# Kernel optimization log

Measured on AMD Instinct MI355X. Metric: run time of the kernel, lower is better.

The kernel has to match this reference:

```python
import jax, jax.numpy as jnp
import numpy as np

B, S, D = 2, 4096, 1024
E, H, TOPK = 8, 2736, 2


def setup_inputs() -> dict:
    key = jax.random.key(0)
    k_x, k_g, k_wg, k_w1, k_w2 = jax.random.split(key, 5)
    scale = 0.02
    return {
        "x": jax.random.normal(k_x, (B, S, D), dtype=jnp.float32),
        "gate_w": jax.random.normal(k_g, (E, D), dtype=jnp.float32) * scale,
        "Wg": jax.random.normal(k_wg, (E, H, D), dtype=jnp.float32) * scale,
        "W1": jax.random.normal(k_w1, (E, H, D), dtype=jnp.float32) * scale,
        "W2": jax.random.normal(k_w2, (E, D, H), dtype=jnp.float32) * scale,
    }


def reference(x, gate_w, Wg, W1, W2):
    C = x.shape[-1]
    xf = x.reshape(-1, C)                     # [T, D], T = B*S tokens
    # --- TopKRouter (eval mode: no jitter) ---
    logits = xf @ gate_w.T                    # [T, E]
    probs = jax.nn.softmax(logits.astype(jnp.float32), axis=-1)
    top_p, top_i = jax.lax.top_k(probs, TOPK)          # [T, K]
    gate_weights = top_p / (top_p.sum(axis=-1, keepdims=True) + 1e-8)
    # combine weight per (token, expert): sum of gate weights over selected slots
    combine = jnp.sum(jax.nn.one_hot(top_i, E, dtype=xf.dtype) * gate_weights[..., None], axis=1)  # [T, E]
    # --- SwiGLU experts, weighted combine ---
    out = jnp.zeros_like(xf)
    for e in range(E):  # fixed small expert count; GEMMs dominate
        g = jax.nn.silu(xf @ Wg[e].T)         # [T, H]
        up = xf @ W1[e].T                     # [T, H]
        y = (g * up) @ W2[e].T                # [T, D]
        out = out + combine[:, e:e + 1] * y
    return out.reshape(x.shape)
```

## Files before the change

kernel.cpp:

```cpp
#include <hip/hip_runtime.h>
#include <hip/hip_bf16.h>
#include <stdint.h>

#define T_TOK 8192
#define DIM   1024
#define NEXP  8
#define HDIM  2736
#define HPAD  2816
#define CAP   16384
#define HB_ROWS 17408

typedef __attribute__((ext_vector_type(8))) short          short8;
typedef __attribute__((ext_vector_type(8))) unsigned short ushort8;
typedef __attribute__((ext_vector_type(4))) float          f32x4;

__device__ __forceinline__ unsigned short f2bf(float f) {
  unsigned u = __float_as_uint(f);
  u = (u + 0x7FFFu + ((u >> 16) & 1u)) >> 16;
  return (unsigned short)u;
}

__device__ __forceinline__ void gld_lds16(const ushort* g, ushort* l) {
  __builtin_amdgcn_global_load_lds((const __attribute__((address_space(1))) uint32_t*)g,
                                   (__attribute__((address_space(3))) uint32_t*)l,
                                   16, 0, 0);
}

__device__ __forceinline__ void stage64(const ushort* __restrict__ src, int ldK,
                                        ushort* lds, int tid) {
#pragma unroll
  for (int i = 0; i < 4; ++i) {
    int c = i * 256 + tid;
    int row = c >> 3, col8 = c & 7;
    gld_lds16(src + (size_t)row * ldK + col8 * 8,
              lds + (size_t)(i * 256 + (tid & 192)) * 8);
  }
}

__global__ void cvt_x_kernel(const float* __restrict__ in, ushort* __restrict__ out, int n8) {
  int i = blockIdx.x * 256 + threadIdx.x;
  if (i >= n8) return;
  const float4* p = (const float4*)in + (size_t)i * 2;
  float4 a = p[0], b = p[1];
  ushort8 v;
  v[0]=f2bf(a.x); v[1]=f2bf(a.y); v[2]=f2bf(a.z); v[3]=f2bf(a.w);
  v[4]=f2bf(b.x); v[5]=f2bf(b.y); v[6]=f2bf(b.z); v[7]=f2bf(b.w);
  ((ushort8*)out)[i] = v;
}

__global__ void cvt_pad_rows_kernel(const float* __restrict__ in, ushort* __restrict__ out, int n8) {
  int i = blockIdx.x * 256 + threadIdx.x;
  if (i >= n8) return;
  int col = i & 127;
  int rowAll = i >> 7;
  int e = rowAll / HPAD;
  int r = rowAll - e * HPAD;
  ushort8 v = (ushort8)0;
  if (r < HDIM) {
    const float4* p = (const float4*)(in + ((size_t)(e * HDIM + r) * DIM + col * 8));
    float4 a = p[0], b = p[1];
    v[0]=f2bf(a.x); v[1]=f2bf(a.y); v[2]=f2bf(a.z); v[3]=f2bf(a.w);
    v[4]=f2bf(b.x); v[5]=f2bf(b.y); v[6]=f2bf(b.z); v[7]=f2bf(b.w);
  }
  ((ushort8*)out)[i] = v;
}

__global__ void cvt_pad_inner_kernel(const float* __restrict__ in, ushort* __restrict__ out, int n8) {
  int i = blockIdx.x * 256 + threadIdx.x;
  if (i >= n8) return;
  int h8 = HPAD / 8;
  int c = i % h8;
  int rowAll = i / h8;
  int h0 = c * 8;
  ushort8 v = (ushort8)0;
  if (h0 < HDIM) {
    const float4* p = (const float4*)(in + (size_t)rowAll * HDIM + h0);
    float4 a = p[0], b = p[1];
    v[0]=f2bf(a.x); v[1]=f2bf(a.y); v[2]=f2bf(a.z); v[3]=f2bf(a.w);
    v[4]=f2bf(b.x); v[5]=f2bf(b.y); v[6]=f2bf(b.z); v[7]=f2bf(b.w);
  }
  ((ushort8*)out)[i] = v;
}

__global__ void topk_kernel(const float* __restrict__ X, const float* __restrict__ GW,
                            int* __restrict__ sel0, int* __restrict__ sel1,
                            float* __restrict__ w0, float* __restrict__ w1) {
  int wave = threadIdx.x >> 6, lane = threadIdx.x & 63;
  int t = blockIdx.x * 4 + wave;
  if (t >= T_TOK) return;
  float acc[NEXP];
#pragma unroll
  for (int e = 0; e < NEXP; ++e) acc[e] = 0.f;
  const float4* xv = (const float4*)(X + (size_t)t * DIM);
#pragma unroll
  for (int it = 0; it < DIM / 4 / 64; ++it) {
    int c = it * 64 + lane;
    float4 xx = xv[c];
#pragma unroll
    for (int e = 0; e < NEXP; ++e) {
      float4 w = ((const float4*)(GW + (size_t)e * DIM))[c];
      acc[e] += xx.x * w.x + xx.y * w.y + xx.z * w.z + xx.w * w.w;
    }
  }
#pragma unroll
  for (int e = 0; e < NEXP; ++e)
#pragma unroll
    for (int off = 32; off > 0; off >>= 1)
      acc[e] += __shfl_down(acc[e], off, 64);
  if (lane == 0) {
    float m = acc[0];
#pragma unroll
    for (int e = 1; e < NEXP; ++e) m = fmaxf(m, acc[e]);
    float p[NEXP], s = 0.f;
#pragma unroll
    for (int e = 0; e < NEXP; ++e) { p[e] = expf(acc[e] - m); s += p[e]; }
#pragma unroll
    for (int e = 0; e < NEXP; ++e) p[e] /= s;
    int i0 = 0;
#pragma unroll
    for (int e = 1; e < NEXP; ++e) if (p[e] > p[i0]) i0 = e;
    int i1 = (i0 == 0) ? 1 : 0;
#pragma unroll
    for (int e = 0; e < NEXP; ++e) if (e != i0 && p[e] > p[i1]) i1 = e;
    float denom = p[i0] + p[i1] + 1e-8f;
    sel0[t] = i0; sel1[t] = i1;
    w0[t] = p[i0] / denom;
    w1[t] = p[i1] / denom;
  }
}

__global__ __launch_bounds__(1024) void build_lists_kernel(
    const int* __restrict__ sel0, const int* __restrict__ sel1,
    int* __restrict__ tok, int* __restrict__ rnk0, int* __restrict__ rnk1,
    int* __restrict__ cnt) {
  int e = blockIdx.x;
  int tid = threadIdx.x;
  int lane = tid & 63, wv = tid >> 6;
  __shared__ int wsum[16], wbase[16], chunktot;
  int base = 0;
  for (int t0 = 0; t0 < T_TOK; t0 += 1024) {
    int t = t0 + tid;
    int s0 = sel0[t], s1 = sel1[t];
    bool isf = (s0 == e);
    bool hit = isf || (s1 == e);
    unsigned long long b = __ballot(hit);
    int rank = __popcll(b & ((1ULL << lane) - 1ULL));
    if (lane == 0) wsum[wv] = __popcll(b);
    __syncthreads();
    if (tid == 0) {
      int s = 0;
#pragma unroll
      for (int w = 0; w < 16; ++w) { wbase[w] = s; s += wsum[w]; }
      chunktot = s;
    }
    __syncthreads();
    if (hit) {
      int pos = base + wbase[wv] + rank;
      tok[e * CAP + pos] = t;
      if (isf) rnk0[t] = pos; else rnk1[t] = pos;
    }
    base += chunktot;
    __syncthreads();
  }
  if (tid == 0) cnt[e] = base;
}

__global__ void offsets_kernel(const int* __restrict__ cnt, int* __restrict__ off) {
  if (threadIdx.x == 0 && blockIdx.x == 0) {
    int o = 0;
#pragma unroll
    for (int e = 0; e < NEXP; ++e) { off[e] = o; o += (cnt[e] + 127) & ~127; }
    off[NEXP] = o;
  }
}

__global__ __launch_bounds__(256) void gemm1_all_kernel(
    const ushort* __restrict__ X,
    const ushort* __restrict__ Wgb,
    const ushort* __restrict__ Wub,
    ushort* __restrict__ Hout,
    const int* __restrict__ tokall,
    const int* __restrict__ cntv, const int* __restrict__ offv) {
  int row0 = blockIdx.x * 128;
  if (row0 >= offv[NEXP]) return;
  int e = 0;
#pragma unroll
  for (int k = 1; k < NEXP; ++k) if (row0 >= offv[k]) e = k;
  int local = row0 - offv[e];
  int cnt = cntv[e];
  const int* tokl = tokall + (size_t)e * CAP;

  __shared__ ushort As[2][128 * 32];
  __shared__ ushort Bg[2][128 * 32];
  __shared__ ushort Bu[2][128 * 32];
  int tid = threadIdx.x;
  int lane = tid & 63, wave = tid >> 6;
  int wr = wave >> 1, wc = wave & 1;
  int lhi = lane >> 4, llo = lane & 15;
  int bcol = blockIdx.y * 128;
  int ldsoff = tid & 192;

  const ushort* asrc[2];
#pragma unroll
  for (int i = 0; i < 2; ++i) {
    int p = local + (tid >> 2) + 64 * i;
    int t = (p < cnt) ? tokl[p] : 0;
    asrc[i] = X + (size_t)t * DIM + (tid & 3) * 8;
  }
  const ushort* Bgb2 = Wgb + (size_t)e * HPAD * DIM + (size_t)bcol * DIM;
  const ushort* Bub2 = Wub + (size_t)e * HPAD * DIM + (size_t)bcol * DIM;
  int brow_b = tid >> 2, bcol8 = tid & 3;

  f32x4 accg[4][4], accu[4][4];
#pragma unroll
  for (int m = 0; m < 4; ++m)
#pragma unroll
    for (int n = 0; n < 4; ++n) { accg[m][n] = (f32x4){0,0,0,0}; accu[m][n] = (f32x4){0,0,0,0}; }

#pragma unroll
  for (int i = 0; i < 2; ++i) {
    int r = brow_b + 64 * i;
    gld_lds16(asrc[i], &As[0][(size_t)(i * 256 + ldsoff) * 8]);
    gld_lds16(Bgb2 + (size_t)r * DIM + bcol8 * 8, &Bg[0][(size_t)(i * 256 + ldsoff) * 8]);
    gld_lds16(Bub2 + (size_t)r * DIM + bcol8 * 8, &Bu[0][(size_t)(i * 256 + ldsoff) * 8]);
  }
  __syncthreads();

  int buf = 0;
  for (int kidx = 0; kidx < DIM / 32; ++kidx) {
    int ko = (kidx + 1) * 32;
    if (ko < DIM) {
      int nb = buf ^ 1;
#pragma unroll
      for (int i = 0; i < 2; ++i) {
        int r = brow_b + 64 * i;
        gld_lds16(asrc[i] + ko, &As[nb][(size_t)(i * 256 + ldsoff) * 8]);
        gld_lds16(Bgb2 + (size_t)r * DIM + ko + bcol8 * 8, &Bg[nb][(size_t)(i * 256 + ldsoff) * 8]);
        gld_lds16(Bub2 + (size_t)r * DIM + ko + bcol8 * 8, &Bu[nb][(size_t)(i * 256 + ldsoff) * 8]);
      }
    }
    const short8* As8 = (const short8*)As[buf];
    const short8* Bg8 = (const short8*)Bg[buf];
    const short8* Bu8 = (const short8*)Bu[buf];
    short8 a[4], bg[4], bu[4];
#pragma unroll
    for (int m = 0; m < 4; ++m)
      a[m] = As8[(wr * 64 + m * 16 + llo) * 4 + lhi];
#pragma unroll
    for (int n = 0; n < 4; ++n) {
      bg[n] = Bg8[(wc * 64 + n * 16 + llo) * 4 + lhi];
      bu[n] = Bu8[(wc * 64 + n * 16 + llo) * 4 + lhi];
    }
#pragma unroll
    for (int m = 0; m < 4; ++m)
#pragma unroll
      for (int n = 0; n < 4; ++n) {
        accg[m][n] = __builtin_amdgcn_mfma_f32_16x16x32_bf16(a[m], bg[n], accg[m][n], 0, 0, 0);
        accu[m][n] = __builtin_amdgcn_mfma_f32_16x16x32_bf16(a[m], bu[n], accu[m][n], 0, 0, 0);
      }
    __syncthreads();
    buf ^= 1;
  }
#pragma unroll
  for (int m = 0; m < 4; ++m)
#pragma unroll
    for (int n = 0; n < 4; ++n)
#pragma unroll
      for (int j = 0; j < 4; ++j) {
        int row = row0 + wr * 64 + m * 16 + lhi * 4 + j;
        int col = bcol + wc * 64 + n * 16 + llo;
        float g = accg[m][n][j];
        float u = accu[m][n][j];
        float h = g / (1.f + __expf(-g)) * u;
        Hout[(size_t)row * HPAD + col] = f2bf(h);
      }
}

__global__ __launch_bounds__(256) void gemm2_all_kernel(
    const ushort* __restrict__ Hin,
    const ushort* __restrict__ W2b,
    float* __restrict__ Yc,
    const int* __restrict__ offv) {
  int row0 = blockIdx.x * 128;
  if (row0 >= offv[NEXP]) return;
  int e = 0;
#pragma unroll
  for (int k = 1; k < NEXP; ++k) if (row0 >= offv[k]) e = k;

  __shared__ ushort As[2][128 * 64];
  __shared__ ushort Bs[2][128 * 64];
  int tid = threadIdx.x;
  int lane = tid & 63, wave = tid >> 6;
  int wr = wave >> 1, wc = wave & 1;
  int lhi = lane >> 4, llo = lane & 15;
  int bcol = blockIdx.y * 128;

  f32x4 acc[4][4];
#pragma unroll
  for (int m = 0; m < 4; ++m)
#pragma unroll
    for (int n = 0; n < 4; ++n) acc[m][n] = (f32x4){0,0,0,0};

  const ushort* Ab = Hin + (size_t)row0 * HPAD;
  const ushort* Bb = W2b + (size_t)e * DIM * HPAD + (size_t)bcol * HPAD;

  stage64(Ab, HPAD, As[0], tid);
  stage64(Bb, HPAD, Bs[0], tid);
  __syncthreads();

  int buf = 0;
  for (int kidx = 0; kidx < HPAD / 64; ++kidx) {
    int ko = (kidx + 1) * 64;
    if (ko < HPAD) {
      int nb = buf ^ 1;
      stage64(Ab + ko, HPAD, As[nb], tid);
      stage64(Bb + ko, HPAD, Bs[nb], tid);
    }
    const short8* As8 = (const short8*)As[buf];
    const short8* Bs8 = (const short8*)Bs[buf];
#pragma unroll
    for (int kk = 0; kk < 2; ++kk) {
      short8 a[4], b[4];
#pragma unroll
      for (int m = 0; m < 4; ++m)
        a[m] = As8[(wr * 64 + m * 16 + llo) * 8 + kk * 4 + lhi];
#pragma unroll
      for (int n = 0; n < 4; ++n)
        b[n] = Bs8[(wc * 64 + n * 16 + llo) * 8 + kk * 4 + lhi];
#pragma unroll
      for (int m = 0; m < 4; ++m)
#pragma unroll
        for (int n = 0; n < 4; ++n)
          acc[m][n] = __builtin_amdgcn_mfma_f32_16x16x32_bf16(a[m], b[n], acc[m][n], 0, 0, 0);
    }
    __syncthreads();
    buf ^= 1;
  }
#pragma unroll
  for (int m = 0; m < 4; ++m)
#pragma unroll
    for (int j = 0; j < 4; ++j) {
      int row = row0 + wr * 64 + m * 16 + lhi * 4 + j;
#pragma unroll
      for (int n = 0; n < 4; ++n) {
        int col = bcol + wc * 64 + n * 16 + llo;
        Yc[(size_t)row * DIM + col] = acc[m][n][j];
      }
    }
}

__global__ __launch_bounds__(256) void combine_kernel(
    const float* __restrict__ Yc,
    const int* __restrict__ sel0, const int* __restrict__ sel1,
    const float* __restrict__ w0, const float* __restrict__ w1,
    const int* __restrict__ rnk0, const int* __restrict__ rnk1,
    const int* __restrict__ offv, float* __restrict__ out) {
  int t = blockIdx.x;
  int c = threadIdx.x;
  int r0 = offv[sel0[t]] + rnk0[t];
  int r1 = offv[sel1[t]] + rnk1[t];
  float a = w0[t], b = w1[t];
  float4 y0 = ((const float4*)(Yc + (size_t)r0 * DIM))[c];
  float4 y1 = ((const float4*)(Yc + (size_t)r1 * DIM))[c];
  float4 o;
  o.x = a * y0.x + b * y1.x;
  o.y = a * y0.y + b * y1.y;
  o.z = a * y0.z + b * y1.z;
  o.w = a * y0.w + b * y1.w;
  ((float4*)(out + (size_t)t * DIM))[c] = o;
}

extern "C" void kernel_launch(void* const* d_in, const int* in_sizes, int n_in,
                              void* d_out, int out_size, void* d_ws, size_t ws_size,
                              hipStream_t stream) {
  const float* x  = (const float*)d_in[0];
  const float* gw = (const float*)d_in[1];
  const float* Wg = (const float*)d_in[2];
  const float* W1 = (const float*)d_in[3];
  const float* W2 = (const float*)d_in[4];
  float* out = (float*)d_out;

  char* p = (char*)d_ws;
  ushort* xb  = (ushort*)p; p += (size_t)T_TOK * DIM * 2;
  ushort* Wgb = (ushort*)p; p += (size_t)NEXP * HPAD * DIM * 2;
  ushort* W1b = (ushort*)p; p += (size_t)NEXP * HPAD * DIM * 2;
  ushort* W2b = (ushort*)p; p += (size_t)NEXP * DIM * HPAD * 2;
  ushort* hb  = (ushort*)p; p += (size_t)HB_ROWS * HPAD * 2;
  int*    tok = (int*)p;    p += (size_t)NEXP * CAP * 4;
  int*   sel0 = (int*)p;    p += T_TOK * 4;
  int*   sel1 = (int*)p;    p += T_TOK * 4;
  float*   w0 = (float*)p;  p += T_TOK * 4;
  float*   w1 = (float*)p;  p += T_TOK * 4;
  int*   rnk0 = (int*)p;    p += T_TOK * 4;
  int*   rnk1 = (int*)p;    p += T_TOK * 4;
  int*    cnt = (int*)p;    p += NEXP * 4;
  int*    off = (int*)p;    p += (NEXP + 1) * 4;
  float*  yc  = (float*)Wgb;

  { int n8 = T_TOK * DIM / 8;
    cvt_x_kernel<<<n8 / 256, 256, 0, stream>>>(x, xb, n8); }
  { int n8 = NEXP * HPAD * DIM / 8;
    cvt_pad_rows_kernel<<<n8 / 256, 256, 0, stream>>>(Wg, Wgb, n8);
    cvt_pad_rows_kernel<<<n8 / 256, 256, 0, stream>>>(W1, W1b, n8);
    cvt_pad_inner_kernel<<<n8 / 256, 256, 0, stream>>>(W2, W2b, n8); }

  topk_kernel<<<T_TOK / 4, 256, 0, stream>>>(x, gw, sel0, sel1, w0, w1);
  build_lists_kernel<<<NEXP, 1024, 0, stream>>>(sel0, sel1, tok, rnk0, rnk1, cnt);
  offsets_kernel<<<1, 64, 0, stream>>>(cnt, off);

  gemm1_all_kernel<<<dim3(HB_ROWS / 128, HPAD / 128), 256, 0, stream>>>(
      xb, Wgb, W1b, hb, tok, cnt, off);
  gemm2_all_kernel<<<dim3(HB_ROWS / 128, DIM / 128), 256, 0, stream>>>(
      hb, W2b, yc, off);
  combine_kernel<<<T_TOK, 256, 0, stream>>>(yc, sel0, sel1, w0, w1, rnk0, rnk1, off, out);
}
```

Baseline: 945.0 us.

## Use 512-thread blocks with XCD-aware tile swizzle in both MoE GEMMs

Both expert GEMM kernels now run 8 waves per 128x128 tile instead of 4. Each wave computes a 64x32 subtile, which halves per-wave accumulators and lets each thread issue fewer global-to-LDS loads per stage. A block-index remap (d&7 stride) spreads consecutive tiles across the 8 XCDs so that tiles sharing the same weight columns are grouped for better L2 reuse. The trade-off is more LDS fragment reads per MFMA, since the A fragments are loaded redundantly by more waves, and more block-wide synchronisation cost.

```diff
diff --git a/kernel.cpp b/kernel.cpp
--- a/kernel.cpp
+++ b/kernel.cpp
@@ -24,17 +24,6 @@
   __builtin_amdgcn_global_load_lds((const __attribute__((address_space(1))) uint32_t*)g,
                                    (__attribute__((address_space(3))) uint32_t*)l,
                                    16, 0, 0);
-}
-
-__device__ __forceinline__ void stage64(const ushort* __restrict__ src, int ldK,
-                                        ushort* lds, int tid) {
-#pragma unroll
-  for (int i = 0; i < 4; ++i) {
-    int c = i * 256 + tid;
-    int row = c >> 3, col8 = c & 7;
-    gld_lds16(src + (size_t)row * ldK + col8 * 8,
-              lds + (size_t)(i * 256 + (tid & 192)) * 8);
-  }
 }
 
 __global__ void cvt_x_kernel(const float* __restrict__ in, ushort* __restrict__ out, int n8) {
@@ -174,14 +163,18 @@
   }
 }
 
-__global__ __launch_bounds__(256) void gemm1_all_kernel(
+__global__ __launch_bounds__(512) void gemm1_all_kernel(
     const ushort* __restrict__ X,
     const ushort* __restrict__ Wgb,
     const ushort* __restrict__ Wub,
     ushort* __restrict__ Hout,
     const int* __restrict__ tokall,
     const int* __restrict__ cntv, const int* __restrict__ offv) {
-  int row0 = blockIdx.x * 128;
+  int d = blockIdx.x + 136 * blockIdx.y;
+  int lid = (d & 7) * (2992 / 8) + (d >> 3);
+  int bx = lid % 136, by = lid / 136;
+
+  int row0 = bx * 128;
   if (row0 >= offv[NEXP]) return;
   int e = 0;
 #pragma unroll
@@ -195,35 +188,26 @@
   __shared__ ushort Bu[2][128 * 32];
   int tid = threadIdx.x;
   int lane = tid & 63, wave = tid >> 6;
-  int wr = wave >> 1, wc = wave & 1;
+  int wr = wave >> 2, wc = wave & 3;
   int lhi = lane >> 4, llo = lane & 15;
-  int bcol = blockIdx.y * 128;
-  int ldsoff = tid & 192;
-
-  const ushort* asrc[2];
-#pragma unroll
-  for (int i = 0; i < 2; ++i) {
-    int p = local + (tid >> 2) + 64 * i;
-    int t = (p < cnt) ? tokl[p] : 0;
-    asrc[i] = X + (size_t)t * DIM + (tid & 3) * 8;
-  }
-  const ushort* Bgb2 = Wgb + (size_t)e * HPAD * DIM + (size_t)bcol * DIM;
-  const ushort* Bub2 = Wub + (size_t)e * HPAD * DIM + (size_t)bcol * DIM;
-  int brow_b = tid >> 2, bcol8 = tid & 3;
-
-  f32x4 accg[4][4], accu[4][4];
+  int bcol = by * 128;
+  int ldsoff8 = (tid & 448) * 8;
+
+  int p = local + (tid >> 2);
+  int t = (p < cnt) ? tokl[p] : 0;
+  const ushort* asrc = X + (size_t)t * DIM + (tid & 3) * 8;
+  const ushort* bgsrc = Wgb + (size_t)e * HPAD * DIM + ((size_t)bcol + (tid >> 2)) * DIM + (tid & 3) * 8;
+  const ushort* busrc = Wub + (size_t)e * HPAD * DIM + ((size_t)bcol + (tid >> 2)) * DIM + (tid & 3) * 8;
+
+  f32x4 accg[4][2], accu[4][2];
 #pragma unroll
   for (int m = 0; m < 4; ++m)
 #pragma unroll
-    for (int n = 0; n < 4; ++n) { accg[m][n] = (f32x4){0,0,0,0}; accu[m][n] = (f32x4){0,0,0,0}; }
-
-#pragma unroll
-  for (int i = 0; i < 2; ++i) {
-    int r = brow_b + 64 * i;
-    gld_lds16(asrc[i], &As[0][(size_t)(i * 256 + ldsoff) * 8]);
-    gld_lds16(Bgb2 + (size_t)r * DIM + bcol8 * 8, &Bg[0][(size_t)(i * 256 + ldsoff) * 8]);
-    gld_lds16(Bub2 + (size_t)r * DIM + bcol8 * 8, &Bu[0][(size_t)(i * 256 + ldsoff) * 8]);
-  }
+    for (int n = 0; n < 2; ++n) { accg[m][n] = (f32x4){0,0,0,0}; accu[m][n] = (f32x4){0,0,0,0}; }
+
+  gld_lds16(asrc,  &As[0][ldsoff8]);
+  gld_lds16(bgsrc, &Bg[0][ldsoff8]);
+  gld_lds16(busrc, &Bu[0][ldsoff8]);
   __syncthreads();
 
   int buf = 0;
@@ -231,30 +215,26 @@
     int ko = (kidx + 1) * 32;
     if (ko < DIM) {
       int nb = buf ^ 1;
-#pragma unroll
-      for (int i = 0; i < 2; ++i) {
-        int r = brow_b + 64 * i;
-        gld_lds16(asrc[i] + ko, &As[nb][(size_t)(i * 256 + ldsoff) * 8]);
-        gld_lds16(Bgb2 + (size_t)r * DIM + ko + bcol8 * 8, &Bg[nb][(size_t)(i * 256 + ldsoff) * 8]);
-        gld_lds16(Bub2 + (size_t)r * DIM + ko + bcol8 * 8, &Bu[nb][(size_t)(i * 256 + ldsoff) * 8]);
-      }
+      gld_lds16(asrc + ko,  &As[nb][ldsoff8]);
+      gld_lds16(bgsrc + ko, &Bg[nb][ldsoff8]);
+      gld_lds16(busrc + ko, &Bu[nb][ldsoff8]);
     }
     const short8* As8 = (const short8*)As[buf];
     const short8* Bg8 = (const short8*)Bg[buf];
     const short8* Bu8 = (const short8*)Bu[buf];
-    short8 a[4], bg[4], bu[4];
+    short8 a[4], bg[2], bu[2];
 #pragma unroll
     for (int m = 0; m < 4; ++m)
       a[m] = As8[(wr * 64 + m * 16 + llo) * 4 + lhi];
 #pragma unroll
-    for (int n = 0; n < 4; ++n) {
-      bg[n] = Bg8[(wc * 64 + n * 16 + llo) * 4 + lhi];
-      bu[n] = Bu8[(wc * 64 + n * 16 + llo) * 4 + lhi];
+    for (int n = 0; n < 2; ++n) {
+      bg[n] = Bg8[(wc * 32 + n * 16 + llo) * 4 + lhi];
+      bu[n] = Bu8[(wc * 32 + n * 16 + llo) * 4 + lhi];
     }
 #pragma unroll
     for (int m = 0; m < 4; ++m)
 #pragma unroll
-      for (int n = 0; n < 4; ++n) {
+      for (int n = 0; n < 2; ++n) {
         accg[m][n] = __builtin_amdgcn_mfma_f32_16x16x32_bf16(a[m], bg[n], accg[m][n], 0, 0, 0);
         accu[m][n] = __builtin_amdgcn_mfma_f32_16x16x32_bf16(a[m], bu[n], accu[m][n], 0, 0, 0);
       }
@@ -264,11 +244,11 @@
 #pragma unroll
   for (int m = 0; m < 4; ++m)
 #pragma unroll
-    for (int n = 0; n < 4; ++n)
+    for (int n = 0; n < 2; ++n)
 #pragma unroll
       for (int j = 0; j < 4; ++j) {
         int row = row0 + wr * 64 + m * 16 + lhi * 4 + j;
-        int col = bcol + wc * 64 + n * 16 + llo;
+        int col = bcol + wc * 32 + n * 16 + llo;
         float g = accg[m][n][j];
         float u = accu[m][n][j];
         float h = g / (1.f + __expf(-g)) * u;
@@ -276,12 +256,16 @@
       }
 }
 
-__global__ __launch_bounds__(256) void gemm2_all_kernel(
+__global__ __launch_bounds__(512) void gemm2_all_kernel(
     const ushort* __restrict__ Hin,
     const ushort* __restrict__ W2b,
     float* __restrict__ Yc,
     const int* __restrict__ offv) {
-  int row0 = blockIdx.x * 128;
+  int d = blockIdx.x + 136 * blockIdx.y;
+  int lid = (d & 7) * (1088 / 8) + (d >> 3);
+  int bx = lid % 136, by = lid / 136;
+
+  int row0 = bx * 128;
   if (row0 >= offv[NEXP]) return;
   int e = 0;
 #pragma unroll
@@ -291,21 +275,25 @@
   __shared__ ushort Bs[2][128 * 64];
   int tid = threadIdx.x;
   int lane = tid & 63, wave = tid >> 6;
-  int wr = wave >> 1, wc = wave & 1;
+  int wr = wave >> 2, wc = wave & 3;
   int lhi = lane >> 4, llo = lane & 15;
-  int bcol = blockIdx.y * 128;
-
-  f32x4 acc[4][4];
+  int bcol = by * 128;
+  int ldsoff8 = (tid & 448) * 8;
+
+  f32x4 acc[4][2];
 #pragma unroll
   for (int m = 0; m < 4; ++m)
 #pragma unroll
-    for (int n = 0; n < 4; ++n) acc[m][n] = (f32x4){0,0,0,0};
-
-  const ushort* Ab = Hin + (size_t)row0 * HPAD;
-  const ushort* Bb = W2b + (size_t)e * DIM * HPAD + (size_t)bcol * HPAD;
-
-  stage64(Ab, HPAD, As[0], tid);
-  stage64(Bb, HPAD, Bs[0], tid);
+    for (int n = 0; n < 2; ++n) acc[m][n] = (f32x4){0,0,0,0};
+
+  const ushort* Ab = Hin + (size_t)row0 * HPAD + (size_t)(tid >> 3) * HPAD + (tid & 7) * 8;
+  const ushort* Bb = W2b + (size_t)e * DIM * HPAD + ((size_t)bcol + (tid >> 3)) * HPAD + (tid & 7) * 8;
+
+#pragma unroll
+  for (int i = 0; i < 2; ++i) {
+    gld_lds16(Ab + (size_t)i * 64 * HPAD, &As[0][(size_t)i * 512 * 8 + ldsoff8]);
+    gld_lds16(Bb + (size_t)i * 64 * HPAD, &Bs[0][(size_t)i * 512 * 8 + ldsoff8]);
+  }
   __syncthreads();
 
   int buf = 0;
@@ -313,24 +301,27 @@
     int ko = (kidx + 1) * 64;
     if (ko < HPAD) {
       int nb = buf ^ 1;
-      stage64(Ab + ko, HPAD, As[nb], tid);
-      stage64(Bb + ko, HPAD, Bs[nb], tid);
+#pragma unroll
+      for (int i = 0; i < 2; ++i) {
+        gld_lds16(Ab + (size_t)i * 64 * HPAD + ko, &As[nb][(size_t)i * 512 * 8 + ldsoff8]);
+        gld_lds16(Bb + (size_t)i * 64 * HPAD + ko, &Bs[nb][(size_t)i * 512 * 8 + ldsoff8]);
+      }
     }
     const short8* As8 = (const short8*)As[buf];
     const short8* Bs8 = (const short8*)Bs[buf];
 #pragma unroll
     for (int kk = 0; kk < 2; ++kk) {
-      short8 a[4], b[4];
+      short8 a[4], b[2];
 #pragma unroll
       for (int m = 0; m < 4; ++m)
         a[m] = As8[(wr * 64 + m * 16 + llo) * 8 + kk * 4 + lhi];
 #pragma unroll
-      for (int n = 0; n < 4; ++n)
-        b[n] = Bs8[(wc * 64 + n * 16 + llo) * 8 + kk * 4 + lhi];
+      for (int n = 0; n < 2; ++n)
+        b[n] = Bs8[(wc * 32 + n * 16 + llo) * 8 + kk * 4 + lhi];
 #pragma unroll
       for (int m = 0; m < 4; ++m)
 #pragma unroll
-        for (int n = 0; n < 4; ++n)
+        for (int n = 0; n < 2; ++n)
           acc[m][n] = __builtin_amdgcn_mfma_f32_16x16x32_bf16(a[m], b[n], acc[m][n], 0, 0, 0);
     }
     __syncthreads();
@@ -342,8 +333,8 @@
     for (int j = 0; j < 4; ++j) {
       int row = row0 + wr * 64 + m * 16 + lhi * 4 + j;
 #pragma unroll
-      for (int n = 0; n < 4; ++n) {
-        int col = bcol + wc * 64 + n * 16 + llo;
+      for (int n = 0; n < 2; ++n) {
+        int col = bcol + wc * 32 + n * 16 + llo;
         Yc[(size_t)row * DIM + col] = acc[m][n][j];
       }
     }
@@ -408,9 +399,9 @@
   build_lists_kernel<<<NEXP, 1024, 0, stream>>>(sel0, sel1, tok, rnk0, rnk1, cnt);
   offsets_kernel<<<1, 64, 0, stream>>>(cnt, off);
 
-  gemm1_all_kernel<<<dim3(HB_ROWS / 128, HPAD / 128), 256, 0, stream>>>(
+  gemm1_all_kernel<<<dim3(HB_ROWS / 128, HPAD / 128), 512, 0, stream>>>(
       xb, Wgb, W1b, hb, tok, cnt, off);
-  gemm2_all_kernel<<<dim3(HB_ROWS / 128, DIM / 128), 256, 0, stream>>>(
+  gemm2_all_kernel<<<dim3(HB_ROWS / 128, DIM / 128), 512, 0, stream>>>(
       hb, W2b, yc, off);
   combine_kernel<<<T_TOK, 256, 0, stream>>>(yc, sel0, sel1, w0, w1, rnk0, rnk1, off, out);
 }
```

Result: faster. 821.4 us (-13.1%).
